# Optimization experiments

Measured on AMD Instinct MI355X. Metric: run time of the kernel, lower is better.

The kernel has to match this reference:

```python
import jax, jax.numpy as jnp
import numpy as np

N = 50_000          # num_nodes
E = 800_000         # num_edges (avg degree 16)
DIMS = [512, 256, 256, 7]   # embedding_dim
SCALING = 2.0


def _glorot(key, shape):
    lim = float(np.sqrt(6.0 / (shape[0] + shape[1])))
    return jax.random.uniform(key, shape, jnp.float32, -lim, lim)


def setup_inputs() -> dict:
    key = jax.random.key(0)
    ks = jax.random.split(key, 16)
    inp = {
        "x": jax.random.normal(ks[0], (N, DIMS[0]), jnp.float32),
        "edge_index": jax.random.randint(ks[1], (2, E), 0, N, dtype=jnp.int32),
        # GCNConv weights (3 layers)
        "W1": _glorot(ks[2], (DIMS[0], DIMS[1])), "b1": jnp.zeros((DIMS[1],), jnp.float32),
        "W2": _glorot(ks[3], (DIMS[1], DIMS[2])), "b2": jnp.zeros((DIMS[2],), jnp.float32),
        "W3": _glorot(ks[4], (DIMS[2], DIMS[3])), "b3": jnp.zeros((DIMS[3],), jnp.float32),
        # pseudo_mlp: Linear(512,512) -> ReLU -> Linear(512,64) -> ReLU -> Linear(64,out)
        "mw1": _glorot(ks[5], (DIMS[0], 512)), "mb1": jnp.zeros((512,), jnp.float32),
        "mw2": _glorot(ks[6], (512, 64)),      "mb2": jnp.zeros((64,), jnp.float32),
        "mw3": _glorot(ks[7], (64, DIMS[-1])), "mb3": jnp.zeros((DIMS[-1],), jnp.float32),
        # parsing_mats[0] (only index 0 is used: learn_soft_edge3 always called with ln=0)
        "parsing0": jnp.ones((DIMS[-1], DIMS[-1]), jnp.float32) / SCALING,
    }
    return inp


def _gcn_conv(h_in, row, col, edge_weight, W, b):
    """PyG-style GCNConv with self-loops, symmetric norm, and per-edge weights."""
    h = h_in @ W                                  # [N, out]
    loop = jnp.arange(N, dtype=row.dtype)
    r = jnp.concatenate([row, loop])
    c = jnp.concatenate([col, loop])
    ew = jnp.concatenate([edge_weight, jnp.ones((N,), h.dtype)])
    deg = jax.ops.segment_sum(ew, c, num_segments=N)
    dinv = jnp.where(deg > 0, jax.lax.rsqrt(jnp.maximum(deg, 1e-12)), 0.0)
    norm = dinv[r] * ew * dinv[c]                 # [E+N]
    out = jax.ops.segment_sum(h[r] * norm[:, None], c, num_segments=N)
    return out + b


def _learn_soft_edge(x, row, col, mw1, mb1, mw2, mb2, mw3, mb3, parsing0):
    # pseudo_mlp logits
    h = jax.nn.relu(x @ mw1 + mb1)
    h = jax.nn.relu(h @ mw2 + mb2)
    logits = h @ mw3 + mb3                        # [N, C]
    s = logits[row]                               # start_logits [E, C]
    e = logits[col]                               # end_logits   [E, C]
    parsing = jax.nn.relu(SCALING * parsing0)     # [C, C]
    # diag(bmm(outer(s,e), P)).sum(-1) == sum_{c,d} s[e,c] * e[e,d] * P[d,c]
    ew = jnp.sum(s * (e @ parsing), axis=1)       # [E]
    mean = ew.mean()
    var = ew.var(ddof=1)                          # torch .var() is unbiased
    return (ew - mean) * jnp.sqrt(1e-4 / var) + 1.0


def reference(x, edge_index, W1, b1, W2, b2, W3, b3,
              mw1, mb1, mw2, mb2, mw3, mb3, parsing0):
    row, col = edge_index[0], edge_index[1]
    ew = _learn_soft_edge(x, row, col, mw1, mb1, mw2, mb2, mw3, mb3, parsing0)
    # layer 0
    h0 = _gcn_conv(x, row, col, ew, W1, b1)       # h = x (saved, pre-ReLU)
    x1 = jax.nn.relu(h0)                          # dropout is identity in eval
    # layer 1 (+ residual to h0)
    x2 = _gcn_conv(x1, row, col, ew, W2, b2)
    x2 = jax.nn.relu(x2) + h0
    # layer 2 (final, no activation)
    out = _gcn_conv(x2, row, col, ew, W3, b3)     # [N, n_classes]
    return out
```

## Files before the change

kernel.cpp:

```cpp
#include <hip/hip_runtime.h>

#define NN 50000
#define EE 800000
#define NB_EDGE 3125
#define NB_SCAN 196

typedef __attribute__((ext_vector_type(4))) float f32x4;
typedef __attribute__((ext_vector_type(8))) short bf16x8;
typedef __attribute__((ext_vector_type(8))) unsigned short u16x8;

typedef const __attribute__((address_space(1))) void* gas_p;
typedef __attribute__((address_space(3))) void* las_p;

__device__ __forceinline__ float bf2f(unsigned short u) {
  union { unsigned int i; float f; } v; v.i = ((unsigned int)u) << 16; return v.f;
}
__device__ __forceinline__ unsigned short f2bf(float f) {
  union { float f; unsigned int i; } v; v.f = f;
  unsigned int u = v.i;
  return (unsigned short)((u + 0x7FFFu + ((u >> 16) & 1u)) >> 16);
}

__device__ __forceinline__ int xcd_swizzle(int orig, int nwg) {
  int xcd = orig & 7;
  int pos = orig >> 3;
  int q = nwg >> 3, r = nwg & 7;
  return (xcd < r ? xcd * (q + 1) : r * (q + 1) + (xcd - r) * q) + pos;
}

constexpr size_t O_XBF  = 0;
constexpr size_t O_H1   = O_XBF + 51200000;
constexpr size_t O_G1   = O_H1  + 51200000;
constexpr size_t O_X1   = O_G1  + 25600000;
constexpr size_t O_H2   = O_X1  + 25600000;
constexpr size_t O_LG   = O_H2  + 6400000;
constexpr size_t O_TG   = O_LG  + 1600000;
constexpr size_t O_EWR  = O_TG  + 1600000;
constexpr size_t O_EWS  = O_EWR + 3200000;
constexpr size_t O_CSR  = O_EWS + 3200000;
constexpr size_t O_MW1T = O_CSR + 6400000;
constexpr size_t O_W1T  = O_MW1T + 524288;
constexpr size_t O_W2T  = O_W1T  + 262144;
constexpr size_t O_MW2T = O_W2T  + 131072;
constexpr size_t O_DEG  = O_MW2T + 65536;
constexpr size_t O_CNT  = O_DEG  + 200192;
constexpr size_t O_CUR  = O_CNT  + 200192;
constexpr size_t O_RED  = O_CUR  + 200192;
constexpr size_t O_RPT  = O_RED  + 256;
constexpr size_t O_DINV = O_RPT  + 200192;
constexpr size_t O_BSUM = O_DINV + 200192;

__global__ __launch_bounds__(256) void conv_f2bf4(const float* __restrict__ in,
                                                  unsigned short* __restrict__ out, int n4) {
  int i = blockIdx.x * 256 + threadIdx.x;
  if (i >= n4) return;
  const float4 v = ((const float4*)in)[i];
  ushort4 o; o.x = f2bf(v.x); o.y = f2bf(v.y); o.z = f2bf(v.z); o.w = f2bf(v.w);
  ((ushort4*)out)[i] = o;
}

__global__ __launch_bounds__(256)
void conv_weights(const float* __restrict__ mw1, const float* __restrict__ W1,
                  const float* __restrict__ W2, const float* __restrict__ mw2,
                  unsigned short* __restrict__ mw1t, unsigned short* __restrict__ w1t,
                  unsigned short* __restrict__ w2t, unsigned short* __restrict__ mw2t)
{
  int i = blockIdx.x * 256 + threadIdx.x;
  if (i < 262144) {
    int k = i >> 9, n = i & 511;
    mw1t[(size_t)n * 512 + k] = f2bf(mw1[i]);
  } else if (i < 393216) {
    int j = i - 262144, k = j >> 8, n = j & 255;
    w1t[(size_t)n * 512 + k] = f2bf(W1[j]);
  } else if (i < 458752) {
    int j = i - 393216, k = j >> 8, n = j & 255;
    w2t[(size_t)n * 256 + k] = f2bf(W2[j]);
  } else if (i < 491520) {
    int j = i - 458752, k = j >> 6, n = j & 63;
    mw2t[(size_t)n * 512 + k] = f2bf(mw2[j]);
  }
}

#define GEMM_BODY(A, lda, Bt, ldb_K, M, Ncols, K, bm, bn)                          \
  __shared__ unsigned short ldsA[128 * 64];                                        \
  __shared__ unsigned short ldsB[128 * 64];                                        \
  const int tid  = threadIdx.x;                                                    \
  const int lane = tid & 63;                                                       \
  const int wid  = tid >> 6;                                                       \
  const int wm   = (wid >> 1) << 6;                                                \
  const int wn   = (wid & 1) << 6;                                                 \
  f32x4 acc[4][4] = {};                                                            \
  const int srow8 = lane >> 3;                                                     \
  const int sks   = (lane & 7) ^ srow8;              \
  for (int k0 = 0; k0 < K; k0 += 64) {                                             \
    if (k0) __syncthreads();                                                       \
    _Pragma("unroll")                                                              \
    for (int r = 0; r < 4; ++r) {                                                  \
      const int row = r * 32 + wid * 8 + srow8;                                    \
      int ga = bm + row; ga = ga < M ? ga : M - 1;                                 \
      int gb = bn + row; gb = gb < Ncols ? gb : Ncols - 1;                         \
      const char* srcA = (const char*)A  + ((size_t)ga * lda + k0) * 2 + sks * 16; \
      const char* srcB = (const char*)Bt + ((size_t)gb * ldb_K + k0) * 2 + sks * 16;\
      __builtin_amdgcn_global_load_lds((gas_p)srcA, (las_p)(ldsA + (r * 32 + wid * 8) * 64), 16, 0, 0); \
      __builtin_amdgcn_global_load_lds((gas_p)srcB, (las_p)(ldsB + (r * 32 + wid * 8) * 64), 16, 0, 0); \
    }                                                                              \
    __syncthreads();                                                               \
    const int q   = lane >> 4;                                                     \
    const int r15 = lane & 15;                                                     \
    _Pragma("unroll")                                                              \
    for (int kk = 0; kk < 2; ++kk) {                                               \
      bf16x8 af[4], bfr[4];                                                        \
      _Pragma("unroll")                                                            \
      for (int m = 0; m < 4; ++m) {                                                \
        const int ra = wm + m * 16 + r15;                                          \
        af[m]  = *(const bf16x8*)(ldsA + ra * 64 + (((kk << 2) + q) ^ (ra & 7)) * 8); \
        const int rb = wn + m * 16 + r15;                                          \
        bfr[m] = *(const bf16x8*)(ldsB + rb * 64 + (((kk << 2) + q) ^ (rb & 7)) * 8); \
      }                                                                            \
      _Pragma("unroll")                                                            \
      for (int m = 0; m < 4; ++m)                                                  \
        _Pragma("unroll")                                                          \
        for (int n = 0; n < 4; ++n)                                                \
          acc[m][n] = __builtin_amdgcn_mfma_f32_16x16x32_bf16(af[m], bfr[n], acc[m][n], 0, 0, 0); \
    }                                                                              \
  }

template<bool RELU, bool BIAS>
__global__ __launch_bounds__(256)
void gemm_bf16(const unsigned short* __restrict__ A, int lda,
               const unsigned short* __restrict__ Bt,
               const float* __restrict__ bias,
               unsigned short* __restrict__ C, int ldc,
               int M, int N, int K)
{
  const int nwg  = gridDim.x * gridDim.y;
  const int wgid = xcd_swizzle(blockIdx.y * gridDim.x + blockIdx.x, nwg);
  const int bn   = (wgid % gridDim.x) << 7;
  const int bm   = (wgid / gridDim.x) << 7;

  GEMM_BODY(A, lda, Bt, K, M, N, K, bm, bn)

  const int q   = lane >> 4;
  const int r15 = lane & 15;
#pragma unroll
  for (int m = 0; m < 4; ++m) {
#pragma unroll
    for (int n = 0; n < 4; ++n) {
      const int gc = bn + wn + n * 16 + r15;
#pragma unroll
      for (int i = 0; i < 4; ++i) {
        const int gr = bm + wm + m * 16 + q * 4 + i;
        if (gr < M && gc < N) {
          float f = acc[m][n][i];
          if (BIAS) f += bias[gc];
          if (RELU) f = fmaxf(f, 0.f);
          C[(size_t)gr * ldc + gc] = f2bf(f);
        }
      }
    }
  }
}

__global__ __launch_bounds__(256)
void gemm_fused(const unsigned short* __restrict__ A,
                const unsigned short* __restrict__ Bt,
                const float* __restrict__ mb1,
                unsigned short* __restrict__ h1,
                unsigned short* __restrict__ g1,
                int M)
{
  const int nwg  = gridDim.x * gridDim.y;
  const int wgid = xcd_swizzle(blockIdx.y * gridDim.x + blockIdx.x, nwg);
  const int bnt  = wgid % gridDim.x;
  const int bn   = bnt << 7;
  const int bm   = (wgid / gridDim.x) << 7;

  GEMM_BODY(A, 512, Bt, 512, M, 768, 512, bm, bn)

  const int q   = lane >> 4;
  const int r15 = lane & 15;
  if (bnt < 4) {
#pragma unroll
    for (int m = 0; m < 4; ++m) {
#pragma unroll
      for (int n = 0; n < 4; ++n) {
        const int gc = bn + wn + n * 16 + r15;
        const float b = mb1[gc];
#pragma unroll
        for (int i = 0; i < 4; ++i) {
          const int gr = bm + wm + m * 16 + q * 4 + i;
          if (gr < M) h1[(size_t)gr * 512 + gc] = f2bf(fmaxf(acc[m][n][i] + b, 0.f));
        }
      }
    }
  } else {
#pragma unroll
    for (int m = 0; m < 4; ++m) {
#pragma unroll
      for (int n = 0; n < 4; ++n) {
        const int gc = bn - 512 + wn + n * 16 + r15;
#pragma unroll
        for (int i = 0; i < 4; ++i) {
          const int gr = bm + wm + m * 16 + q * 4 + i;
          if (gr < M) g1[(size_t)gr * 256 + gc] = f2bf(acc[m][n][i]);
        }
      }
    }
  }
}

__global__ __launch_bounds__(256)
void logits_kernel(const unsigned short* __restrict__ h2, const float* __restrict__ mw3,
                   const float* __restrict__ mb3, const float* __restrict__ par,
                   float* __restrict__ Lg, float* __restrict__ Tg)
{
  __shared__ float w[64 * 8];
  __shared__ float P[64];
  int tid = threadIdx.x;
  for (int i = tid; i < 512; i += 256) {
    int k = i >> 3, c = i & 7;
    w[i] = (c < 7) ? mw3[k * 7 + c] : 0.f;
  }
  if (tid < 64) {
    int d = tid >> 3, c = tid & 7;
    P[tid] = (d < 7 && c < 7) ? fmaxf(2.0f * par[d * 7 + c], 0.f) : 0.f;
  }
  __syncthreads();
  int n = blockIdx.x * 256 + tid;
  if (n >= NN) return;
  const unsigned short* hr = h2 + (size_t)n * 64;
  f32x4 L0 = {0,0,0,0}, L1 = {0,0,0,0};
  for (int k = 0; k < 64; k += 4) {
    ushort4 v = *(const ushort4*)(hr + k);
    float xs[4] = {bf2f(v.x), bf2f(v.y), bf2f(v.z), bf2f(v.w)};
#pragma unroll
    for (int j = 0; j < 4; ++j) {
      L0 += xs[j] * *(const f32x4*)&w[(k + j) * 8];
      L1 += xs[j] * *(const f32x4*)&w[(k + j) * 8 + 4];
    }
  }
  float Ls[8] = {L0[0], L0[1], L0[2], L0[3], L1[0], L1[1], L1[2], 0.f};
#pragma unroll
  for (int c = 0; c < 7; ++c) Ls[c] += mb3[c];
  f32x4 T0 = {0,0,0,0}, T1 = {0,0,0,0};
#pragma unroll
  for (int d = 0; d < 7; ++d) {
    T0 += Ls[d] * *(const f32x4*)&P[d * 8];
    T1 += Ls[d] * *(const f32x4*)&P[d * 8 + 4];
  }
  f32x4 o0 = {Ls[0], Ls[1], Ls[2], Ls[3]};
  f32x4 o1 = {Ls[4], Ls[5], Ls[6], 0.f};
  *(f32x4*)(Lg + (size_t)n * 8)     = o0;
  *(f32x4*)(Lg + (size_t)n * 8 + 4) = o1;
  *(f32x4*)(Tg + (size_t)n * 8)     = T0;
  *(f32x4*)(Tg + (size_t)n * 8 + 4) = T1;
}

__global__ __launch_bounds__(256)
void edge1_kernel(const int* __restrict__ row, const int* __restrict__ col,
                  const float* __restrict__ Lg, const float* __restrict__ Tg,
                  float* __restrict__ ew_raw, int* __restrict__ cnt,
                  double* __restrict__ part)
{
  __shared__ double shs[4], shs2[4];
  int e = blockIdx.x * 256 + threadIdx.x;
  double s = 0.0, s2 = 0.0;
  if (e < EE) {
    int r = row[e], c = col[e];
    float4 a0 = *(const float4*)(Lg + (size_t)r * 8);
    float4 a1 = *(const float4*)(Lg + (size_t)r * 8 + 4);
    float4 b0 = *(const float4*)(Tg + (size_t)c * 8);
    float4 b1 = *(const float4*)(Tg + (size_t)c * 8 + 4);
    float v = a0.x*b0.x + a0.y*b0.y + a0.z*b0.z + a0.w*b0.w
            + a1.x*b1.x + a1.y*b1.y + a1.z*b1.z + a1.w*b1.w;
    ew_raw[e] = v;
    atomicAdd(&cnt[c], 1);
    s = (double)v; s2 = (double)v * (double)v;
  }
  for (int off = 32; off; off >>= 1) {
    s  += __shfl_down(s, off);
    s2 += __shfl_down(s2, off);
  }
  int wv = threadIdx.x >> 6;
  if ((threadIdx.x & 63) == 0) { shs[wv] = s; shs2[wv] = s2; }
  __syncthreads();
  if (threadIdx.x == 0) {
    part[blockIdx.x]           = shs[0] + shs[1] + shs[2] + shs[3];
    part[NB_EDGE + blockIdx.x] = shs2[0] + shs2[1] + shs2[2] + shs2[3];
  }
}

__global__ __launch_bounds__(1024)
void redpart_kernel(const double* __restrict__ part, double* __restrict__ red)
{
  __shared__ double sh[16][2];
  int tid = threadIdx.x;
  double s = 0.0, s2 = 0.0;
  for (int i = tid; i < NB_EDGE; i += 1024) {
    s  += part[i];
    s2 += part[NB_EDGE + i];
  }
  for (int off = 32; off; off >>= 1) {
    s  += __shfl_down(s, off);
    s2 += __shfl_down(s2, off);
  }
  if ((tid & 63) == 0) { sh[tid >> 6][0] = s; sh[tid >> 6][1] = s2; }
  __syncthreads();
  if (tid == 0) {
    double a = 0.0, b = 0.0;
    for (int i = 0; i < 16; ++i) { a += sh[i][0]; b += sh[i][1]; }
    red[0] = a; red[1] = b;
  }
}

__global__ __launch_bounds__(256)
void edge2_kernel(const float* __restrict__ ew_raw, const int* __restrict__ col,
                  const double* __restrict__ red,
                  float* __restrict__ ew_std, float* __restrict__ deg)
{
  int e = blockIdx.x * 256 + threadIdx.x;
  if (e >= EE) return;
  double mean = red[0] / (double)EE;
  double var  = (red[1] - (double)EE * mean * mean) / (double)(EE - 1);
  double scl  = sqrt(1e-4 / var);
  float v = (float)(((double)ew_raw[e] - mean) * scl) + 1.0f;
  ew_std[e] = v;
  atomicAdd(&deg[col[e]], v);
}

__global__ __launch_bounds__(256)
void dinv_kernel(const float* __restrict__ deg, float* __restrict__ dinv)
{
  int n = blockIdx.x * 256 + threadIdx.x;
  if (n >= NN) return;
  float d = deg[n] + 1.0f;
  dinv[n] = d > 0.f ? 1.0f / sqrtf(fmaxf(d, 1e-12f)) : 0.f;
}

__global__ __launch_bounds__(256)
void scan1_kernel(const int* __restrict__ cnt, int* __restrict__ bsum)
{
  __shared__ int sh[4];
  int i = blockIdx.x * 256 + threadIdx.x;
  int v = (i < NN) ? cnt[i] : 0;
  for (int off = 32; off; off >>= 1) v += __shfl_down(v, off);
  if ((threadIdx.x & 63) == 0) sh[threadIdx.x >> 6] = v;
  __syncthreads();
  if (threadIdx.x == 0) bsum[blockIdx.x] = sh[0] + sh[1] + sh[2] + sh[3];
}

__global__ __launch_bounds__(256)
void scan2_kernel(int* __restrict__ bsum)
{
  __shared__ int sh[256];
  int tid = threadIdx.x;
  int v = (tid < NB_SCAN) ? bsum[tid] : 0;
  sh[tid] = v;
  __syncthreads();
  for (int off = 1; off < 256; off <<= 1) {
    int t = (tid >= off) ? sh[tid - off] : 0;
    __syncthreads();
    sh[tid] += t;
    __syncthreads();
  }
  if (tid < NB_SCAN) bsum[tid] = sh[tid] - v;
}

__global__ __launch_bounds__(256)
void scan3_kernel(const int* __restrict__ cnt, const int* __restrict__ bsum,
                  int* __restrict__ rowptr)
{
  __shared__ int sh[256];
  int tid = threadIdx.x;
  int i = blockIdx.x * 256 + tid;
  int v = (i < NN) ? cnt[i] : 0;
  sh[tid] = v;
  __syncthreads();
  for (int off = 1; off < 256; off <<= 1) {
    int t = (tid >= off) ? sh[tid - off] : 0;
    __syncthreads();
    sh[tid] += t;
    __syncthreads();
  }
  if (i < NN) rowptr[i + 1] = bsum[blockIdx.x] + sh[tid];
  if (i == 0) rowptr[0] = 0;
}

__global__ __launch_bounds__(256)
void edge3_kernel(const int* __restrict__ row, const int* __restrict__ col,
                  const float* __restrict__ ew_std, const float* __restrict__ dinv,
                  const int* __restrict__ rowptr, int* __restrict__ cursor,
                  int2* __restrict__ csr_sw)
{
  int e = blockIdx.x * 256 + threadIdx.x;
  if (e >= EE) return;
  int r = row[e], c = col[e];
  float w = dinv[r] * ew_std[e] * dinv[c];
  int pos = atomicAdd(&cursor[c], 1);
  int2 sw; sw.x = r; sw.y = __float_as_int(w);
  csr_sw[rowptr[c] + pos] = sw;
}

template<int MODE>
__global__ __launch_bounds__(256)
void agg256_kernel(const int* __restrict__ rowptr, const int2* __restrict__ csr_sw,
                   const unsigned short* __restrict__ gsrc,
                   const float* __restrict__ dinv, const float* __restrict__ bias,
                   const unsigned short* __restrict__ h0in,
                   unsigned short* __restrict__ h0out,
                   unsigned short* __restrict__ xout)
{
  int n = blockIdx.x * 4 + (threadIdx.x >> 6);
  if (n >= NN) return;
  const int lane = threadIdx.x & 63;
  const int half = lane >> 5;
  const int l5   = lane & 31;
  const size_t colbase = (size_t)(l5 << 3);

  float a0=0,a1=0,a2=0,a3=0,a4=0,a5=0,a6=0,a7=0;
  const int s = rowptr[n], e = rowptr[n + 1];
  int i = s + half;
  for (; i + 6 < e; i += 8) {
    int2 sw0 = csr_sw[i];
    int2 sw1 = csr_sw[i + 2];
    int2 sw2 = csr_sw[i + 4];
    int2 sw3 = csr_sw[i + 6];
    u16x8 v0 = *(const u16x8*)(gsrc + (size_t)sw0.x * 256 + colbase);
    u16x8 v1 = *(const u16x8*)(gsrc + (size_t)sw1.x * 256 + colbase);
    u16x8 v2 = *(const u16x8*)(gsrc + (size_t)sw2.x * 256 + colbase);
    u16x8 v3 = *(const u16x8*)(gsrc + (size_t)sw3.x * 256 + colbase);
    float w0 = __int_as_float(sw0.y);
    float w1 = __int_as_float(sw1.y);
    float w2 = __int_as_float(sw2.y);
    float w3 = __int_as_float(sw3.y);
    a0 += w0 * bf2f(v0[0]); a1 += w0 * bf2f(v0[1]);
    a2 += w0 * bf2f(v0[2]); a3 += w0 * bf2f(v0[3]);
    a4 += w0 * bf2f(v0[4]); a5 += w0 * bf2f(v0[5]);
    a6 += w0 * bf2f(v0[6]); a7 += w0 * bf2f(v0[7]);
    a0 += w1 * bf2f(v1[0]); a1 += w1 * bf2f(v1[1]);
    a2 += w1 * bf2f(v1[2]); a3 += w1 * bf2f(v1[3]);
    a4 += w1 * bf2f(v1[4]); a5 += w1 * bf2f(v1[5]);
    a6 += w1 * bf2f(v1[6]); a7 += w1 * bf2f(v1[7]);
    a0 += w2 * bf2f(v2[0]); a1 += w2 * bf2f(v2[1]);
    a2 += w2 * bf2f(v2[2]); a3 += w2 * bf2f(v2[3]);
    a4 += w2 * bf2f(v2[4]); a5 += w2 * bf2f(v2[5]);
    a6 += w2 * bf2f(v2[6]); a7 += w2 * bf2f(v2[7]);
    a0 += w3 * bf2f(v3[0]); a1 += w3 * bf2f(v3[1]);
    a2 += w3 * bf2f(v3[2]); a3 += w3 * bf2f(v3[3]);
    a4 += w3 * bf2f(v3[4]); a5 += w3 * bf2f(v3[5]);
    a6 += w3 * bf2f(v3[6]); a7 += w3 * bf2f(v3[7]);
  }
  for (; i < e; i += 2) {
    int2 sw = csr_sw[i];
    u16x8 v = *(const u16x8*)(gsrc + (size_t)sw.x * 256 + colbase);
    float w = __int_as_float(sw.y);
    a0 += w * bf2f(v[0]); a1 += w * bf2f(v[1]);
    a2 += w * bf2f(v[2]); a3 += w * bf2f(v[3]);
    a4 += w * bf2f(v[4]); a5 += w * bf2f(v[5]);
    a6 += w * bf2f(v[6]); a7 += w * bf2f(v[7]);
  }
  a0 += __shfl_xor(a0, 32); a1 += __shfl_xor(a1, 32);
  a2 += __shfl_xor(a2, 32); a3 += __shfl_xor(a3, 32);
  a4 += __shfl_xor(a4, 32); a5 += __shfl_xor(a5, 32);
  a6 += __shfl_xor(a6, 32); a7 += __shfl_xor(a7, 32);
  float f0 = half ? a4 : a0;
  float f1 = half ? a5 : a1;
  float f2 = half ? a6 : a2;
  float f3 = half ? a7 : a3;
  const int dbase = (l5 << 3) + (half << 2);
  float wd = dinv[n]; wd *= wd;
  ushort4 sv = *(const ushort4*)(gsrc + (size_t)n * 256 + dbase);
  f0 += wd * bf2f(sv.x); f1 += wd * bf2f(sv.y);
  f2 += wd * bf2f(sv.z); f3 += wd * bf2f(sv.w);
  float4 b = *(const float4*)(bias + dbase);
  f0 += b.x; f1 += b.y; f2 += b.z; f3 += b.w;
  const size_t o = (size_t)n * 256 + dbase;
  if (MODE == 0) {
    ushort4 h;
    h.x = f2bf(f0); h.y = f2bf(f1); h.z = f2bf(f2); h.w = f2bf(f3);
    *(ushort4*)(h0out + o) = h;
    ushort4 xo;
    xo.x = f2bf(fmaxf(f0, 0.f)); xo.y = f2bf(fmaxf(f1, 0.f));
    xo.z = f2bf(fmaxf(f2, 0.f)); xo.w = f2bf(fmaxf(f3, 0.f));
    *(ushort4*)(xout + o) = xo;
  } else {
    ushort4 h = *(const ushort4*)(h0in + o);
    ushort4 xo;
    xo.x = f2bf(fmaxf(f0, 0.f) + bf2f(h.x));
    xo.y = f2bf(fmaxf(f1, 0.f) + bf2f(h.y));
    xo.z = f2bf(fmaxf(f2, 0.f) + bf2f(h.z));
    xo.w = f2bf(fmaxf(f3, 0.f) + bf2f(h.w));
    *(ushort4*)(xout + o) = xo;
  }
}

__global__ __launch_bounds__(256)
void gemv7_kernel(const unsigned short* __restrict__ x2, const float* __restrict__ W3,
                  float* __restrict__ y3)
{
  __shared__ float w[256 * 8];
  int tid = threadIdx.x;
  for (int i = tid; i < 2048; i += 256) {
    int k = i >> 3, c = i & 7;
    w[i] = (c < 7) ? W3[k * 7 + c] : 0.f;
  }
  __syncthreads();
  int n = blockIdx.x * 256 + tid;
  if (n >= NN) return;
  const unsigned short* xr = x2 + (size_t)n * 256;
  f32x4 accLo = {0,0,0,0}, accHi = {0,0,0,0};
  for (int k = 0; k < 256; k += 4) {
    ushort4 v = *(const ushort4*)(xr + k);
    float xs[4] = {bf2f(v.x), bf2f(v.y), bf2f(v.z), bf2f(v.w)};
#pragma unroll
    for (int j = 0; j < 4; ++j) {
      accLo += xs[j] * *(const f32x4*)&w[(k + j) * 8];
      accHi += xs[j] * *(const f32x4*)&w[(k + j) * 8 + 4];
    }
  }
  *(f32x4*)(y3 + (size_t)n * 8)     = accLo;
  *(f32x4*)(y3 + (size_t)n * 8 + 4) = accHi;
}

__global__ __launch_bounds__(256)
void agg7_kernel(const int* __restrict__ rowptr, const int2* __restrict__ csr_sw,
                 const float* __restrict__ y3,
                 const float* __restrict__ dinv, const float* __restrict__ b3,
                 float* __restrict__ out)
{
  int n = blockIdx.x * 32 + (threadIdx.x >> 3);
  if (n >= NN) return;
  int j = threadIdx.x & 7;
  float acc = 0.f;
  int s = rowptr[n], e = rowptr[n + 1];
  for (int i = s; i < e; ++i) {
    int2 sw = csr_sw[i];
    acc += __int_as_float(sw.y) * y3[(size_t)sw.x * 8 + j];
  }
  float wd = dinv[n]; wd *= wd;
  acc += wd * y3[(size_t)n * 8 + j];
  if (j < 7) out[(size_t)n * 7 + j] = acc + b3[j];
}

extern "C" void kernel_launch(void* const* d_in, const int* in_sizes, int n_in,
                              void* d_out, int out_size, void* d_ws, size_t ws_size,
                              hipStream_t stream)
{
  const float* x   = (const float*)d_in[0];
  const int*   ei  = (const int*)d_in[1];
  const float* W1  = (const float*)d_in[2];
  const float* b1  = (const float*)d_in[3];
  const float* W2  = (const float*)d_in[4];
  const float* b2  = (const float*)d_in[5];
  const float* W3  = (const float*)d_in[6];
  const float* b3  = (const float*)d_in[7];
  const float* mw1 = (const float*)d_in[8];
  const float* mb1 = (const float*)d_in[9];
  const float* mw2 = (const float*)d_in[10];
  const float* mb2 = (const float*)d_in[11];
  const float* mw3 = (const float*)d_in[12];
  const float* mb3 = (const float*)d_in[13];
  const float* par = (const float*)d_in[14];
  const int* row = ei;
  const int* col = ei + EE;
  float* out = (float*)d_out;

  char* ws = (char*)d_ws;
  unsigned short* x_bf  = (unsigned short*)(ws + O_XBF);
  unsigned short* h0    = (unsigned short*)(ws + O_XBF);
  unsigned short* h1_bf = (unsigned short*)(ws + O_H1);
  unsigned short* g2_bf = (unsigned short*)(ws + O_H1);
  unsigned short* x2_bf = (unsigned short*)(ws + O_H1 + 25600000);
  unsigned short* g1_bf = (unsigned short*)(ws + O_G1);
  unsigned short* x1_bf = (unsigned short*)(ws + O_X1);
  unsigned short* h2_bf = (unsigned short*)(ws + O_H2);
  float* Lg      = (float*)(ws + O_LG);
  float* Tg      = (float*)(ws + O_TG);
  float* ew_raw  = (float*)(ws + O_EWR);
  float* y3      = (float*)(ws + O_EWR);
  float* ew_std  = (float*)(ws + O_EWS);
  int2*  csr_sw  = (int2*)(ws + O_CSR);
  double* part   = (double*)(ws + O_CSR);
  unsigned short* mw1t = (unsigned short*)(ws + O_MW1T);
  unsigned short* w1t  = (unsigned short*)(ws + O_W1T);
  unsigned short* w2t  = (unsigned short*)(ws + O_W2T);
  unsigned short* mw2t = (unsigned short*)(ws + O_MW2T);
  float*  deg    = (float*)(ws + O_DEG);
  int*    cnt    = (int*)(ws + O_CNT);
  int*    cursor = (int*)(ws + O_CUR);
  double* red    = (double*)(ws + O_RED);
  int*    rowptr = (int*)(ws + O_RPT);
  float*  dinv   = (float*)(ws + O_DINV);
  int*    bsum   = (int*)(ws + O_BSUM);

  hipMemsetAsync(ws + O_DEG, 0, 3 * 200192, stream);

  conv_f2bf4<<<25000, 256, 0, stream>>>(x, x_bf, NN * 512 / 4);
  conv_weights<<<1920, 256, 0, stream>>>(mw1, W1, W2, mw2, mw1t, w1t, w2t, mw2t);

  gemm_fused<<<dim3(6, 391), 256, 0, stream>>>(x_bf, mw1t, mb1, h1_bf, g1_bf, NN);
  gemm_bf16<true,  true ><<<dim3(1, 391), 256, 0, stream>>>(h1_bf, 512, mw2t, mb2, h2_bf, 64, NN, 64, 512);
  logits_kernel<<<196, 256, 0, stream>>>(h2_bf, mw3, mb3, par, Lg, Tg);

  edge1_kernel<<<NB_EDGE, 256, 0, stream>>>(row, col, Lg, Tg, ew_raw, cnt, part);
  redpart_kernel<<<1, 1024, 0, stream>>>(part, red);
  edge2_kernel<<<NB_EDGE, 256, 0, stream>>>(ew_raw, col, red, ew_std, deg);
  dinv_kernel<<<196, 256, 0, stream>>>(deg, dinv);
  scan1_kernel<<<NB_SCAN, 256, 0, stream>>>(cnt, bsum);
  scan2_kernel<<<1, 256, 0, stream>>>(bsum);
  scan3_kernel<<<NB_SCAN, 256, 0, stream>>>(cnt, bsum, rowptr);
  edge3_kernel<<<NB_EDGE, 256, 0, stream>>>(row, col, ew_std, dinv, rowptr, cursor, csr_sw);

  agg256_kernel<0><<<12500, 256, 0, stream>>>(rowptr, csr_sw, g1_bf, dinv, b1, nullptr, h0, x1_bf);
  gemm_bf16<false, false><<<dim3(2, 391), 256, 0, stream>>>(x1_bf, 256, w2t, nullptr, g2_bf, 256, NN, 256, 256);
  agg256_kernel<1><<<12500, 256, 0, stream>>>(rowptr, csr_sw, g2_bf, dinv, b2, h0, nullptr, x2_bf);
  gemv7_kernel<<<196, 256, 0, stream>>>(x2_bf, W3, y3);
  agg7_kernel<<<1563, 256, 0, stream>>>(rowptr, csr_sw, y3, dinv, b3, out);
}
```

Measured before the change: 447.8 us.

## Double-buffer GEMM LDS tiles and deepen gather unroll in aggregation

The bf16 GEMM now uses two LDS buffers per operand. The next K-tile's global_load_lds is issued before computing on the current one, with explicit vmcnt waits and raw s_barrier replacing __syncthreads, so load latency can overlap MFMA work. The aggregation kernel adds a 16-edge unrolled loop that issues 8 independent row gathers per half-wave, raising memory-level parallelism. The cost is double the LDS footprint, which can lower occupancy, plus higher register pressure in the aggregation kernel. The hand-counted vmcnt(8) relies on exactly 8 loads per stage.

Result: no change. 453.3 us (+1.2%).

```diff
diff --git a/kernel.cpp b/kernel.cpp
--- a/kernel.cpp
+++ b/kernel.cpp
@@ -81,9 +81,24 @@
   }
 }
 
+#define GEMM_STAGE(buf, k0)                                                        \
+  _Pragma("unroll")                                                                \
+  for (int r = 0; r < 4; ++r) {                                                    \
+    const int row = r * 32 + wid * 8 + srow8;                                      \
+    int ga = bm + row; ga = ga < M_ ? ga : M_ - 1;                                 \
+    int gb = bn + row; gb = gb < N_ ? gb : N_ - 1;                                 \
+    __builtin_amdgcn_global_load_lds((gas_p)(pA_ + ((size_t)ga * lda_ + (k0)) * 2 + sks * 16), \
+                                     (las_p)(ldsA[buf] + row * 64), 16, 0, 0);     \
+    __builtin_amdgcn_global_load_lds((gas_p)(pB_ + ((size_t)gb * ldb_ + (k0)) * 2 + sks * 16), \
+                                     (las_p)(ldsB[buf] + row * 64), 16, 0, 0);     \
+  }
+
 #define GEMM_BODY(A, lda, Bt, ldb_K, M, Ncols, K, bm, bn)                          \
-  __shared__ unsigned short ldsA[128 * 64];                                        \
-  __shared__ unsigned short ldsB[128 * 64];                                        \
+  __shared__ unsigned short ldsA[2][128 * 64];                                     \
+  __shared__ unsigned short ldsB[2][128 * 64];                                     \
+  const char* pA_ = (const char*)(A);                                              \
+  const char* pB_ = (const char*)(Bt);                                             \
+  const int lda_ = (lda), ldb_ = (ldb_K), M_ = (M), N_ = (Ncols);                  \
   const int tid  = threadIdx.x;                                                    \
   const int lane = tid & 63;                                                       \
   const int wid  = tid >> 6;                                                       \
@@ -91,20 +106,19 @@
   const int wn   = (wid & 1) << 6;                                                 \
   f32x4 acc[4][4] = {};                                                            \
   const int srow8 = lane >> 3;                                                     \
-  const int sks   = (lane & 7) ^ srow8;              \
-  for (int k0 = 0; k0 < K; k0 += 64) {                                             \
-    if (k0) __syncthreads();                                                       \
-    _Pragma("unroll")                                                              \
-    for (int r = 0; r < 4; ++r) {                                                  \
-      const int row = r * 32 + wid * 8 + srow8;                                    \
-      int ga = bm + row; ga = ga < M ? ga : M - 1;                                 \
-      int gb = bn + row; gb = gb < Ncols ? gb : Ncols - 1;                         \
-      const char* srcA = (const char*)A  + ((size_t)ga * lda + k0) * 2 + sks * 16; \
-      const char* srcB = (const char*)Bt + ((size_t)gb * ldb_K + k0) * 2 + sks * 16;\
-      __builtin_amdgcn_global_load_lds((gas_p)srcA, (las_p)(ldsA + (r * 32 + wid * 8) * 64), 16, 0, 0); \
-      __builtin_amdgcn_global_load_lds((gas_p)srcB, (las_p)(ldsB + (r * 32 + wid * 8) * 64), 16, 0, 0); \
+  const int sks   = (lane & 7) ^ srow8;                                            \
+  const int nt    = (K) >> 6;                                                      \
+  GEMM_STAGE(0, 0)                                                                 \
+  for (int t = 0; t < nt; ++t) {                                                   \
+    const int cur = t & 1;                                                         \
+    if (t + 1 < nt) {                                                              \
+      GEMM_STAGE(cur ^ 1, (t + 1) << 6)                                            \
+      asm volatile("s_waitcnt vmcnt(8)" ::: "memory");                             \
+    } else {                                                                       \
+      asm volatile("s_waitcnt vmcnt(0)" ::: "memory");                             \
     }                                                                              \
-    __syncthreads();                                                               \
+    __builtin_amdgcn_s_barrier();                                                  \
+    __builtin_amdgcn_sched_barrier(0);                                             \
     const int q   = lane >> 4;                                                     \
     const int r15 = lane & 15;                                                     \
     _Pragma("unroll")                                                              \
@@ -113,9 +127,9 @@
       _Pragma("unroll")                                                            \
       for (int m = 0; m < 4; ++m) {                                                \
         const int ra = wm + m * 16 + r15;                                          \
-        af[m]  = *(const bf16x8*)(ldsA + ra * 64 + (((kk << 2) + q) ^ (ra & 7)) * 8); \
+        af[m]  = *(const bf16x8*)(ldsA[cur] + ra * 64 + (((kk << 2) + q) ^ (ra & 7)) * 8); \
         const int rb = wn + m * 16 + r15;                                          \
-        bfr[m] = *(const bf16x8*)(ldsB + rb * 64 + (((kk << 2) + q) ^ (rb & 7)) * 8); \
+        bfr[m] = *(const bf16x8*)(ldsB[cur] + rb * 64 + (((kk << 2) + q) ^ (rb & 7)) * 8); \
       }                                                                            \
       _Pragma("unroll")                                                            \
       for (int m = 0; m < 4; ++m)                                                  \
@@ -123,6 +137,8 @@
         for (int n = 0; n < 4; ++n)                                                \
           acc[m][n] = __builtin_amdgcn_mfma_f32_16x16x32_bf16(af[m], bfr[n], acc[m][n], 0, 0, 0); \
     }                                                                              \
+    __builtin_amdgcn_sched_barrier(0);                                             \
+    __builtin_amdgcn_s_barrier();                                                  \
   }
 
 template<bool RELU, bool BIAS>
@@ -401,6 +417,15 @@
   csr_sw[rowptr[c] + pos] = sw;
 }
 
+#define AGG_ACC(sw_, v_)                                                     \
+  {                                                                          \
+    float w_ = __int_as_float((sw_).y);                                      \
+    a0 += w_ * bf2f((v_)[0]); a1 += w_ * bf2f((v_)[1]);                      \
+    a2 += w_ * bf2f((v_)[2]); a3 += w_ * bf2f((v_)[3]);                      \
+    a4 += w_ * bf2f((v_)[4]); a5 += w_ * bf2f((v_)[5]);                      \
+    a6 += w_ * bf2f((v_)[6]); a7 += w_ * bf2f((v_)[7]);                      \
+  }
+
 template<int MODE>
 __global__ __launch_bounds__(256)
 void agg256_kernel(const int* __restrict__ rowptr, const int2* __restrict__ csr_sw,
@@ -420,44 +445,30 @@
   float a0=0,a1=0,a2=0,a3=0,a4=0,a5=0,a6=0,a7=0;
   const int s = rowptr[n], e = rowptr[n + 1];
   int i = s + half;
+  for (; i + 14 < e; i += 16) {
+    int2 sw[8];
+#pragma unroll
+    for (int u = 0; u < 8; ++u) sw[u] = csr_sw[i + 2 * u];
+    u16x8 v[8];
+#pragma unroll
+    for (int u = 0; u < 8; ++u) v[u] = *(const u16x8*)(gsrc + (size_t)sw[u].x * 256 + colbase);
+#pragma unroll
+    for (int u = 0; u < 8; ++u) AGG_ACC(sw[u], v[u])
+  }
   for (; i + 6 < e; i += 8) {
-    int2 sw0 = csr_sw[i];
-    int2 sw1 = csr_sw[i + 2];
-    int2 sw2 = csr_sw[i + 4];
-    int2 sw3 = csr_sw[i + 6];
-    u16x8 v0 = *(const u16x8*)(gsrc + (size_t)sw0.x * 256 + colbase);
-    u16x8 v1 = *(const u16x8*)(gsrc + (size_t)sw1.x * 256 + colbase);
-    u16x8 v2 = *(const u16x8*)(gsrc + (size_t)sw2.x * 256 + colbase);
-    u16x8 v3 = *(const u16x8*)(gsrc + (size_t)sw3.x * 256 + colbase);
-    float w0 = __int_as_float(sw0.y);
-    float w1 = __int_as_float(sw1.y);
-    float w2 = __int_as_float(sw2.y);
-    float w3 = __int_as_float(sw3.y);
-    a0 += w0 * bf2f(v0[0]); a1 += w0 * bf2f(v0[1]);
-    a2 += w0 * bf2f(v0[2]); a3 += w0 * bf2f(v0[3]);
-    a4 += w0 * bf2f(v0[4]); a5 += w0 * bf2f(v0[5]);
-    a6 += w0 * bf2f(v0[6]); a7 += w0 * bf2f(v0[7]);
-    a0 += w1 * bf2f(v1[0]); a1 += w1 * bf2f(v1[1]);
-    a2 += w1 * bf2f(v1[2]); a3 += w1 * bf2f(v1[3]);
-    a4 += w1 * bf2f(v1[4]); a5 += w1 * bf2f(v1[5]);
-    a6 += w1 * bf2f(v1[6]); a7 += w1 * bf2f(v1[7]);
-    a0 += w2 * bf2f(v2[0]); a1 += w2 * bf2f(v2[1]);
-    a2 += w2 * bf2f(v2[2]); a3 += w2 * bf2f(v2[3]);
-    a4 += w2 * bf2f(v2[4]); a5 += w2 * bf2f(v2[5]);
-    a6 += w2 * bf2f(v2[6]); a7 += w2 * bf2f(v2[7]);
-    a0 += w3 * bf2f(v3[0]); a1 += w3 * bf2f(v3[1]);
-    a2 += w3 * bf2f(v3[2]); a3 += w3 * bf2f(v3[3]);
-    a4 += w3 * bf2f(v3[4]); a5 += w3 * bf2f(v3[5]);
-    a6 += w3 * bf2f(v3[6]); a7 += w3 * bf2f(v3[7]);
+    int2 sw[4];
+#pragma unroll
+    for (int u = 0; u < 4; ++u) sw[u] = csr_sw[i + 2 * u];
+    u16x8 v[4];
+#pragma unroll
+    for (int u = 0; u < 4; ++u) v[u] = *(const u16x8*)(gsrc + (size_t)sw[u].x * 256 + colbase);
+#pragma unroll
+    for (int u = 0; u < 4; ++u) AGG_ACC(sw[u], v[u])
   }
   for (; i < e; i += 2) {
     int2 sw = csr_sw[i];
     u16x8 v = *(const u16x8*)(gsrc + (size_t)sw.x * 256 + colbase);
-    float w = __int_as_float(sw.y);
-    a0 += w * bf2f(v[0]); a1 += w * bf2f(v[1]);
-    a2 += w * bf2f(v[2]); a3 += w * bf2f(v[3]);
-    a4 += w * bf2f(v[4]); a5 += w * bf2f(v[5]);
-    a6 += w * bf2f(v[6]); a7 += w * bf2f(v[7]);
+    AGG_ACC(sw, v)
   }
   a0 += __shfl_xor(a0, 32); a1 += __shfl_xor(a1, 32);
   a2 += __shfl_xor(a2, 32); a3 += __shfl_xor(a3, 32);
```
